# Optimization experiments

Hardware: AMD Instinct MI355X
Metric: run time of the kernel (lower is better)

Reference implementation:

```python
import jax, jax.numpy as jnp
import numpy as np

# Problem dims (match init_kwargs)
M, P, TINI, NH, TT, NB = 4, 6, 50, 100, 2000, 4096
L = TT - TINI - NH + 1  # 1851, dimension of g
NC = TINI * M + TINI * P + P  # 506 equality constraints
DELTA = 1e-6  # tiny ridge on g so the KKT system is nonsingular (u,y unchanged to ~1e-6)


def block_hankel(w, Lr, d):
    """w: flat [T*d] time series (d-dim samples stacked). Returns [Lr*d, T-Lr+1].
    H[d*i+k, j] = w[d*(i+j)+k] = w[row + d*j]."""
    T = w.shape[0] // d
    cols = T - Lr + 1
    return w[jnp.arange(Lr * d)[:, None] + d * jnp.arange(cols)[None, :]]


def setup_inputs() -> dict:
    key = jax.random.key(0)
    ks = jax.random.split(key, 7)
    ud = jax.random.normal(ks[0], (TT, M), jnp.float32)          # input data series
    yd = jax.random.normal(ks[1], (TT, P), jnp.float32)          # output data series
    q = 10.0 + 0.1 * jax.random.normal(ks[2], (P * NH,), jnp.float32)  # diag of Q (positive)
    r = 10.0 + 0.1 * jax.random.normal(ks[3], (M * NH,), jnp.float32)  # diag of R (positive)
    ref = jax.random.normal(ks[4], (NB, NH * P), jnp.float32)
    u_ini = jax.random.normal(ks[5], (NB, TINI * M), jnp.float32)
    y_ini = jax.random.normal(ks[6], (NB, TINI * P), jnp.float32)
    return {"ud": ud, "yd": yd, "q": q, "r": r, "ref": ref, "u_ini": u_ini, "y_ini": y_ini}


def reference(ud, yd, q, r, ref, u_ini, y_ini):
    # Block-Hankel data matrices (the module's U, Y Parameters)
    U = block_hankel(ud.reshape(-1), TINI + NH, M)  # [(Tini+N)*m, L]
    Y = block_hankel(yd.reshape(-1), TINI + NH, P)  # [(Tini+N)*p, L]
    Up, Uf = U[: M * TINI], U[M * TINI:]            # [Tini*m, L], [N*m, L]
    Yp, Yf = Y[: P * TINI], Y[P * TINI:]            # [Tini*p, L], [N*p, L]

    # Deterministic (linear, non-stochastic) DeePC QP with inactive box constraints:
    #   min_g (Yf g - ref)^T Q (Yf g - ref) + (Uf g)^T R (Uf g)
    #   s.t.  Up g = u_ini, Yp g = y_ini, (Yf g)[-p:] = ref[-p:]
    # Solved exactly via the KKT system (unique in u = Uf g, y = Yf g).
    H = Yf.T @ (q[:, None] * Yf) + Uf.T @ (r[:, None] * Uf) + DELTA * jnp.eye(L, dtype=ud.dtype)
    A = jnp.concatenate([Up, Yp, Yf[-P:]], axis=0)  # [NC, L]
    KKT = jnp.block([
        [2.0 * H, A.T],
        [A, jnp.zeros((NC, NC), dtype=ud.dtype)],
    ])  # [L+NC, L+NC]

    rhs = jnp.concatenate([
        2.0 * (Yf.T @ (q[:, None] * ref.T)),  # [L, NB] gradient term
        u_ini.T,                               # [Tini*m, NB]
        y_ini.T,                               # [Tini*p, NB]
        ref[:, -P:].T,                          # [p, NB] terminal constraint
    ], axis=0)

    g = jnp.linalg.solve(KKT, rhs)[:L]  # [L, NB]
    inp = Uf @ g   # optimal input  [N*m, NB]
    out = Yf @ g   # optimal output [N*p, NB]
    return inp, out
```

## Files before the change

kernel.cpp:

```cpp
#include <hip/hip_runtime.h>
#include <hip/hip_bf16.h>

#define LDIM   1851
#define NFR    1000
#define NAR    506
#define NCRP   1536
#define LDC    1856
#define NG     1024
#define NS     512
#define NXC    1152
#define LDMA   1120
#define NBATCH 4096
#define NOUT   1000
#define INVDP  500000.0

#define OFF_C     ((size_t)0)
#define SZ_C      ((size_t)NCRP * LDC * 4)
#define OFF_ILG   OFF_C
#define OFF_ILS   (OFF_C + 8388608)
#define OFF_GCC   (OFF_C + SZ_C)
#define SZ_GCC    ((size_t)NCRP * NCRP * 8)
#define OFF_G     (OFF_GCC + SZ_GCC)
#define SZ_G      ((size_t)NG * NG * 8)
#define OFF_TA    (OFF_G + SZ_G)
#define SZ_TA     ((size_t)NG * NS * 8)
#define OFF_S     (OFF_TA + SZ_TA)
#define SZ_S      ((size_t)NS * NS * 8)
#define OFF_X12   (OFF_S + SZ_S)
#define SZ_X12    ((size_t)NS * NXC * 8)
#define OFF_MRAW  (OFF_X12 + SZ_X12)
#define SZ_MRAW   ((size_t)NG * NXC * 4)
#define OFF_XB    OFF_MRAW
#define OFF_MALL  (OFF_MRAW + SZ_MRAW)
#define SZ_MALL   ((size_t)NG * LDMA * 4)
#define OFF_IDG   OFF_MALL
#define OFF_IDS   (OFF_MALL + 524288)
#define OFF_WG    (OFF_MALL + 786432)
#define OFF_WS    (OFF_MALL + 1310720)
#define OFF_LS    (OFF_MALL + 1572864)
#define OFF_INALL (OFF_MALL + SZ_MALL)
#define SZ_INALL  ((size_t)LDMA * NBATCH * 4)
#define OFF_TB    OFF_INALL
#define OFF_TINV  (OFF_INALL + 4194304)
#define OFF_LG    (OFF_INALL + 6291456)

__device__ __forceinline__ double dweight(int i, const float* q, const float* r) {
  return (i < 400) ? (double)r[i] : (double)q[i - 400];
}

__global__ __launch_bounds__(256) void k_build_C(const float* __restrict__ ud,
                                                 const float* __restrict__ yd,
                                                 float* __restrict__ C) {
  int j = blockIdx.x * 256 + threadIdx.x;
  int rr = blockIdx.y;
  if (j >= LDC) return;
  float v = 0.f;
  if (j < LDIM) {
    if (rr < 400)        v = ud[200 + rr + 4 * j];
    else if (rr < 1000)  v = yd[300 + (rr - 400) + 6 * j];
    else if (rr < 1200)  v = ud[(rr - 1000) + 4 * j];
    else if (rr < 1500)  v = yd[(rr - 1200) + 6 * j];
    else if (rr < 1506)  v = yd[894 + (rr - 1500) + 6 * j];
  }
  C[(size_t)rr * LDC + j] = v;
}

__global__ __launch_bounds__(256) void k_gram(const float* __restrict__ C,
                                              double* __restrict__ GCC) {
  int ti = blockIdx.y;
  int tj = blockIdx.x;
  if (ti * 32 + 31 < tj * 64) return;
  __shared__ float As[32][33];
  __shared__ float Bs[64][33];
  int tid = threadIdx.x;
  int tr2 = (tid >> 4) * 2, tc4 = (tid & 15) * 4;
  double acc[2][4] = {};
  int i0 = ti * 32, j0 = tj * 64;
  for (int k0 = 0; k0 < LDC; k0 += 32) {
#pragma unroll
    for (int l = 0; l < 4; ++l) {
      int t = tid + l * 256;
      As[t >> 5][t & 31] = C[(size_t)(i0 + (t >> 5)) * LDC + k0 + (t & 31)];
    }
#pragma unroll
    for (int l = 0; l < 8; ++l) {
      int t = tid + l * 256;
      Bs[t >> 5][t & 31] = C[(size_t)(j0 + (t >> 5)) * LDC + k0 + (t & 31)];
    }
    __syncthreads();
#pragma unroll
    for (int kk = 0; kk < 32; ++kk) {
      double a[2], b[4];
#pragma unroll
      for (int i = 0; i < 2; ++i) a[i] = (double)As[tr2 + i][kk];
#pragma unroll
      for (int jx = 0; jx < 4; ++jx) b[jx] = (double)Bs[tc4 + jx][kk];
#pragma unroll
      for (int i = 0; i < 2; ++i)
#pragma unroll
        for (int jx = 0; jx < 4; ++jx) acc[i][jx] += a[i] * b[jx];
    }
    __syncthreads();
  }
#pragma unroll
  for (int i = 0; i < 2; ++i)
#pragma unroll
    for (int jx = 0; jx < 4; ++jx) {
      int gi = i0 + tr2 + i, gj = j0 + tc4 + jx;
      GCC[(size_t)gi * NCRP + gj] = acc[i][jx];
      if (gi > gj) GCC[(size_t)gj * NCRP + gi] = acc[i][jx];
    }
}

__global__ __launch_bounds__(256) void k_copyG(const double* __restrict__ GCC,
                                               const float* __restrict__ q,
                                               const float* __restrict__ r,
                                               double* __restrict__ G) {
  int idx = blockIdx.x * 256 + threadIdx.x;
  int i = idx >> 10, j = idx & 1023;
  double v = (i < NFR && j < NFR) ? GCC[(size_t)i * NCRP + j] : 0.0;
  if (i == j) {
    if (i < NFR) v += 1e-6 / dweight(i, q, r);
    else v = 1.0;
  }
  G[idx] = v;
}

__global__ __launch_bounds__(256) void k_copyTA(const double* __restrict__ GCC,
                                                double* __restrict__ TA) {
  int idx = blockIdx.x * 256 + threadIdx.x;
  int f = idx >> 9, a = idx & 511;
  TA[idx] = (f < NFR && a < NAR) ? GCC[(size_t)f * NCRP + 1000 + a] : 0.0;
}

__device__ __forceinline__ void potrf_inv_w(double* sm, int tid,
                                            double* Ldst, int ld,
                                            double* iLout, double* Wout) {
  double* invd = sm + 4160;
  for (int c = 0; c < 64; ++c) {
    if (tid == 0) sm[c * 65 + c] = sqrt(sm[c * 65 + c]);
    __syncthreads();
    double piv = sm[c * 65 + c];
    for (int rr = c + 1 + tid; rr < 64; rr += 256) sm[rr * 65 + c] /= piv;
    __syncthreads();
    for (int t = tid; t < 64 * 64; t += 256) {
      int rr = t >> 6, jj = t & 63;
      if (rr > c && jj > c) sm[rr * 65 + jj] -= sm[rr * 65 + c] * sm[jj * 65 + c];
    }
    __syncthreads();
  }
#pragma unroll
  for (int l = 0; l < 16; ++l) {
    int t = tid + l * 256;
    Ldst[(size_t)(t >> 6) * ld + (t & 63)] = sm[(t >> 6) * 65 + (t & 63)];
  }
  __syncthreads();
  if (tid < 64) invd[tid] = 1.0 / sm[tid * 65 + tid];
  __syncthreads();
  if (tid < 64) {
    int c = tid;
    for (int r = c + 1; r < 64; ++r) {
      double s = sm[r * 65 + c] * invd[c];
      for (int j = c + 1; j < r; ++j) s += sm[r * 65 + j] * sm[c * 65 + j];
      sm[c * 65 + r] = -s * invd[r];
    }
  }
  __syncthreads();
#pragma unroll
  for (int l = 0; l < 16; ++l) {
    int t = tid + l * 256;
    int r = t >> 6, c = t & 63;
    iLout[t] = (r < c) ? 0.0 : (r == c ? invd[r] : sm[c * 65 + r]);
  }
  for (int idx = tid; idx < 4096; idx += 256) {
    int r = idx >> 6, c = idx & 63;
    int k2 = r > c ? r : c;
    double s = 0.0;
    for (; k2 < 64; ++k2) {
      double ar = (k2 == r) ? invd[r] : sm[r * 65 + k2];
      double ac = (k2 == c) ? invd[c] : sm[c * 65 + k2];
      s += ar * ac;
    }
    Wout[idx] = s;
  }
}

__global__ __launch_bounds__(256) void k_potrf_inv0(double* __restrict__ M, int ld,
                                                    double* __restrict__ LG,
                                                    double* __restrict__ iL0,
                                                    double* __restrict__ W0) {
  __shared__ double sm[4160 + 64];
  int tid = threadIdx.x;
#pragma unroll
  for (int l = 0; l < 16; ++l) {
    int t = tid + l * 256;
    sm[(t >> 6) * 65 + (t & 63)] = M[(size_t)(t >> 6) * ld + (t & 63)];
  }
  __syncthreads();
  potrf_inv_w(sm, tid, LG, ld, iL0, W0);
}

#define FS1(r, c) sm[(r) * 65 + (c)]
#define FS2(r, c) sm[4160 + (r) * 33 + (c)]
__global__ __launch_bounds__(256) void k_chol_fused(double* __restrict__ M, int ld, int k,
                                                    const double* __restrict__ iLcur,
                                                    const double* __restrict__ Wcur,
                                                    double* __restrict__ LG,
                                                    double* __restrict__ iLnext,
                                                    double* __restrict__ Wnext) {
  __shared__ double sm[6272];
  int tid = threadIdx.x;
  int t = blockIdx.x;
  int i = (int)((sqrtf(8.f * t + 1.f) - 1.f) * 0.5f);
  while ((i + 1) * (i + 2) / 2 <= t) ++i;
  while (i * (i + 1) / 2 > t) --i;
  int j = t - i * (i + 1) / 2;
  int tr4 = (tid >> 4) * 4, tc4 = (tid & 15) * 4;
  int rowAi = k + 64 + i * 64, rowAj = k + 64 + j * 64;

  if (j == 0) {
#pragma unroll
    for (int l = 0; l < 16; ++l) { int t2 = tid + l * 256; FS1(t2 >> 6, t2 & 63) = iLcur[t2]; }
    __syncthreads();
    double li[4][4] = {};
    for (int k0 = 0; k0 < 64; k0 += 32) {
#pragma unroll
      for (int l = 0; l < 8; ++l) {
        int t2 = tid + l * 256;
        FS2(t2 >> 5, t2 & 31) = M[(size_t)(rowAi + (t2 >> 5)) * ld + k + k0 + (t2 & 31)];
      }
      __syncthreads();
#pragma unroll
      for (int mm = 0; mm < 32; ++mm) {
        double a[4], b[4];
#pragma unroll
        for (int i2 = 0; i2 < 4; ++i2) a[i2] = FS2(tr4 + i2, mm);
#pragma unroll
        for (int j2 = 0; j2 < 4; ++j2) b[j2] = FS1(tc4 + j2, k0 + mm);
#pragma unroll
        for (int i2 = 0; i2 < 4; ++i2)
#pragma unroll
          for (int j2 = 0; j2 < 4; ++j2) li[i2][j2] += a[i2] * b[j2];
      }
      __syncthreads();
    }
#pragma unroll
    for (int i2 = 0; i2 < 4; ++i2)
#pragma unroll
      for (int j2 = 0; j2 < 4; ++j2)
        LG[(size_t)(rowAi + tr4 + i2) * ld + k + tc4 + j2] = li[i2][j2];
  }
  __syncthreads();

#pragma unroll
  for (int l = 0; l < 16; ++l) { int t2 = tid + l * 256; FS1(t2 >> 6, t2 & 63) = Wcur[t2]; }
  __syncthreads();
  double acc[4][4] = {};
  for (int k0 = 0; k0 < 64; k0 += 32) {
#pragma unroll
    for (int l = 0; l < 8; ++l) {
      int t2 = tid + l * 256;
      FS2(t2 >> 5, t2 & 31) = M[(size_t)(rowAj + (t2 >> 5)) * ld + k + k0 + (t2 & 31)];
    }
    __syncthreads();
#pragma unroll
    for (int mm = 0; mm < 32; ++mm) {
      double a[4], b[4];
#pragma unroll
      for (int i2 = 0; i2 < 4; ++i2) a[i2] = FS1(tr4 + i2, k0 + mm);
#pragma unroll
      for (int j2 = 0; j2 < 4; ++j2) b[j2] = FS2(tc4 + j2, mm);
#pragma unroll
      for (int i2 = 0; i2 < 4; ++i2)
#pragma unroll
        for (int j2 = 0; j2 < 4; ++j2) acc[i2][j2] += a[i2] * b[j2];
    }
    __syncthreads();
  }
#pragma unroll
  for (int i2 = 0; i2 < 4; ++i2)
#pragma unroll
    for (int j2 = 0; j2 < 4; ++j2) FS1(tr4 + i2, tc4 + j2) = acc[i2][j2];
  __syncthreads();
  double acc2[4][4] = {};
  for (int k0 = 0; k0 < 64; k0 += 32) {
#pragma unroll
    for (int l = 0; l < 8; ++l) {
      int t2 = tid + l * 256;
      FS2(t2 >> 5, t2 & 31) = M[(size_t)(rowAi + (t2 >> 5)) * ld + k + k0 + (t2 & 31)];
    }
    __syncthreads();
#pragma unroll
    for (int mm = 0; mm < 32; ++mm) {
      double a[4], b[4];
#pragma unroll
      for (int i2 = 0; i2 < 4; ++i2) a[i2] = FS2(tr4 + i2, mm);
#pragma unroll
      for (int j2 = 0; j2 < 4; ++j2) b[j2] = FS1(k0 + mm, tc4 + j2);
#pragma unroll
      for (int i2 = 0; i2 < 4; ++i2)
#pragma unroll
        for (int j2 = 0; j2 < 4; ++j2) acc2[i2][j2] += a[i2] * b[j2];
    }
    __syncthreads();
  }
  double upd[4][4];
#pragma unroll
  for (int i2 = 0; i2 < 4; ++i2)
#pragma unroll
    for (int j2 = 0; j2 < 4; ++j2) {
      size_t off = (size_t)(rowAi + tr4 + i2) * ld + rowAj + tc4 + j2;
      upd[i2][j2] = M[off] - acc2[i2][j2];
      M[off] = upd[i2][j2];
    }

  if (blockIdx.x == 0) {
    __syncthreads();
#pragma unroll
    for (int i2 = 0; i2 < 4; ++i2)
#pragma unroll
      for (int j2 = 0; j2 < 4; ++j2) FS1(tr4 + i2, tc4 + j2) = upd[i2][j2];
    __syncthreads();
    potrf_inv_w(sm, tid, LG + (size_t)(k + 64) * ld + (k + 64), ld, iLnext, Wnext);
  }
}

__device__ __forceinline__ void dgemm_nn_core(const double* __restrict__ A, int lda,
                                              const double* __restrict__ B, int ldb,
                                              double* __restrict__ C, int ldc,
                                              int kBeg, int kEnd, double alpha) {
  __shared__ double As[64][33];
  __shared__ double Bs[32][65];
  int tid = threadIdx.x;
  int tr4 = (tid >> 4) * 4, tc4 = (tid & 15) * 4;
  double acc[4][4] = {};
  for (int k0 = kBeg; k0 < kEnd; k0 += 32) {
#pragma unroll
    for (int l = 0; l < 8; ++l) {
      int t = tid + l * 256;
      As[t >> 5][t & 31] = A[(size_t)(t >> 5) * lda + k0 + (t & 31)];
    }
#pragma unroll
    for (int l = 0; l < 8; ++l) {
      int t = tid + l * 256;
      Bs[t >> 6][t & 63] = B[(size_t)(k0 + (t >> 6)) * ldb + (t & 63)];
    }
    __syncthreads();
#pragma unroll
    for (int kk = 0; kk < 32; ++kk) {
      double a[4], b[4];
#pragma unroll
      for (int i = 0; i < 4; ++i) a[i] = As[tr4 + i][kk];
#pragma unroll
      for (int jx = 0; jx < 4; ++jx) b[jx] = Bs[kk][tc4 + jx];
#pragma unroll
      for (int i = 0; i < 4; ++i)
#pragma unroll
        for (int jx = 0; jx < 4; ++jx) acc[i][jx] += a[i] * b[jx];
    }
    __syncthreads();
  }
#pragma unroll
  for (int i = 0; i < 4; ++i)
#pragma unroll
    for (int jx = 0; jx < 4; ++jx)
      C[(size_t)(tr4 + i) * ldc + tc4 + jx] = alpha * acc[i][jx];
}

__device__ __forceinline__ void dgemm_tn_core(const double* __restrict__ A, int lda,
                                              const double* __restrict__ B, int ldb,
                                              double* __restrict__ C, int ldc,
                                              int kBeg, int kEnd, double alpha) {
  __shared__ double Ls[32][65];
  __shared__ double Bs[32][65];
  int tid = threadIdx.x;
  int tr4 = (tid >> 4) * 4, tc4 = (tid & 15) * 4;
  double acc[4][4] = {};
  for (int k0 = kBeg; k0 < kEnd; k0 += 32) {
#pragma unroll
    for (int l = 0; l < 8; ++l) {
      int t = tid + l * 256;
      int jj = t >> 6, rr = t & 63;
      Ls[jj][rr] = A[(size_t)(k0 + jj) * lda + rr];
    }
#pragma unroll
    for (int l = 0; l < 8; ++l) {
      int t = tid + l * 256;
      Bs[t >> 6][t & 63] = B[(size_t)(k0 + (t >> 6)) * ldb + (t & 63)];
    }
    __syncthreads();
#pragma unroll
    for (int kk = 0; kk < 32; ++kk) {
      double a[4], b[4];
#pragma unroll
      for (int i = 0; i < 4; ++i) a[i] = Ls[kk][tr4 + i];
#pragma unroll
      for (int jx = 0; jx < 4; ++jx) b[jx] = Bs[kk][tc4 + jx];
#pragma unroll
      for (int i = 0; i < 4; ++i)
#pragma unroll
        for (int jx = 0; jx < 4; ++jx) acc[i][jx] += a[i] * b[jx];
    }
    __syncthreads();
  }
#pragma unroll
  for (int i = 0; i < 4; ++i)
#pragma unroll
    for (int jx = 0; jx < 4; ++jx)
      C[(size_t)(tr4 + i) * ldc + tc4 + jx] = alpha * acc[i][jx];
}

__global__ __launch_bounds__(256) void k_dgemm_nn(const double* __restrict__ A, int lda,
                                                  const double* __restrict__ B, int ldb,
                                                  double* __restrict__ C, int ldc,
                                                  int K, int tri, double alpha) {
  int bi = blockIdx.y, bj = blockIdx.x;
  int kEnd = tri ? ((bi + 1) * 64 < K ? (bi + 1) * 64 : K) : K;
  dgemm_nn_core(A + (size_t)bi * 64 * lda, lda, B + bj * 64, ldb,
                C + (size_t)bi * 64 * ldc + bj * 64, ldc, 0, kEnd, alpha);
}

__global__ __launch_bounds__(256) void k_dgemm_tn(const double* __restrict__ A, int lda,
                                                  const double* __restrict__ B, int ldb,
                                                  double* __restrict__ C, int ldc,
                                                  int K, int tri, double alpha) {
  int bi = blockIdx.y, bj = blockIdx.x;
  int kBeg = tri ? bi * 64 : 0;
  dgemm_tn_core(A + bi * 64, lda, B + bj * 64, ldb,
                C + (size_t)bi * 64 * ldc + bj * 64, ldc, kBeg, K, alpha);
}

__global__ __launch_bounds__(256) void k_init_iL(double* __restrict__ iL, int nShift,
                                                 const double* __restrict__ IDIAG) {
  int idx = blockIdx.x * 256 + threadIdx.x;
  int n = 1 << nShift;
  int i = idx >> nShift, j = idx & (n - 1);
  int d = i >> 6;
  double v = 0.0;
  if ((j >> 6) == d) v = IDIAG[(size_t)d * 4096 + (i & 63) * 64 + (j & 63)];
  iL[idx] = v;
}

__global__ __launch_bounds__(256) void k_ilv_tmp(const double* __restrict__ L, int ldl,
                                                 const double* __restrict__ iL, int ldi,
                                                 double* __restrict__ T, int half) {
  int p = blockIdx.z, bi = blockIdx.y, bj = blockIdx.x;
  int base = p * 2 * half;
  dgemm_nn_core(L + (size_t)(base + half + bi * 64) * ldl + base, ldl,
                iL + (size_t)base * ldi + base + bj * 64, ldi,
                T + (size_t)p * half * half + (size_t)bi * 64 * half + bj * 64, half,
                0, half, 1.0);
}

__global__ __launch_bounds__(256) void k_ilv_fin(double* __restrict__ iL, int ldi,
                                                 const double* __restrict__ T, int half) {
  int p = blockIdx.z, bi = blockIdx.y, bj = blockIdx.x;
  int base = p * 2 * half;
  dgemm_nn_core(iL + (size_t)(base + half + bi * 64) * ldi + base + half, ldi,
                T + (size_t)p * half * half + bj * 64, half,
                iL + (size_t)(base + half + bi * 64) * ldi + base + bj * 64, ldi,
                0, half, -1.0);
}

__global__ __launch_bounds__(256) void k_buildS(const double* __restrict__ GCC,
                                                const double* __restrict__ TA,
                                                double* __restrict__ S) {
  __shared__ double Ga[64][33];
  __shared__ double Tb[32][65];
  int tid = threadIdx.x;
  int tr4 = (tid >> 4) * 4, tc4 = (tid & 15) * 4;
  int a0 = blockIdx.y * 64, b0 = blockIdx.x * 64;
  double acc[4][4] = {};
  for (int f0 = 0; f0 < NG; f0 += 32) {
#pragma unroll
    for (int l = 0; l < 8; ++l) {
      int t = tid + l * 256;
      Ga[t >> 5][t & 31] = GCC[(size_t)(1000 + a0 + (t >> 5)) * NCRP + f0 + (t & 31)];
    }
#pragma unroll
    for (int l = 0; l < 8; ++l) {
      int t = tid + l * 256;
      Tb[t >> 6][t & 63] = TA[(size_t)(f0 + (t >> 6)) * NS + b0 + (t & 63)];
    }
    __syncthreads();
#pragma unroll
    for (int kk = 0; kk < 32; ++kk) {
      double a[4], b[4];
#pragma unroll
      for (int i = 0; i < 4; ++i) a[i] = Ga[tr4 + i][kk];
#pragma unroll
      for (int jx = 0; jx < 4; ++jx) b[jx] = Tb[kk][tc4 + jx];
#pragma unroll
      for (int i = 0; i < 4; ++i)
#pragma unroll
        for (int jx = 0; jx < 4; ++jx) acc[i][jx] += a[i] * b[jx];
    }
    __syncthreads();
  }
#pragma unroll
  for (int i = 0; i < 4; ++i)
#pragma unroll
    for (int jx = 0; jx < 4; ++jx) {
      int a = a0 + tr4 + i, b = b0 + tc4 + jx;
      double v;
      if (a < NAR && b < NAR)
        v = (GCC[(size_t)(1000 + a) * NCRP + 1000 + b] - acc[i][jx]) * INVDP;
      else
        v = (a == b) ? 1.0 : 0.0;
      S[(size_t)a * NS + b] = v;
    }
}

__global__ __launch_bounds__(256) void k_build_x12rhs(const double* __restrict__ TA,
                                                      double* __restrict__ X12) {
  int c = blockIdx.x * 256 + threadIdx.x;
  int a = blockIdx.y;
  if (c >= NXC) return;
  double v = 0.0;
  if (a < NAR) {
    if (c < 600) v = TA[(size_t)(400 + c) * NS + a];
    else if (c < 1106) v = (a == (c - 600)) ? 1.0 : 0.0;
  }
  X12[(size_t)a * NXC + c] = v;
}

__global__ __launch_bounds__(256) void k_gemm_M(const double* __restrict__ TA,
                                                const double* __restrict__ X12,
                                                const float* __restrict__ q,
                                                const float* __restrict__ r,
                                                float* __restrict__ Mraw) {
  __shared__ double Ga[64][33];
  __shared__ double Xb[32][65];
  int tid = threadIdx.x;
  int tr4 = (tid >> 4) * 4, tc4 = (tid & 15) * 4;
  int o0 = blockIdx.y * 64, c0 = blockIdx.x * 64;
  double acc[4][4] = {};
  for (int k0 = 0; k0 < NS; k0 += 32) {
#pragma unroll
    for (int l = 0; l < 8; ++l) {
      int t = tid + l * 256;
      Ga[t >> 5][t & 31] = TA[(size_t)(o0 + (t >> 5)) * NS + k0 + (t & 31)];
    }
#pragma unroll
    for (int l = 0; l < 8; ++l) {
      int t = tid + l * 256;
      Xb[t >> 6][t & 63] = X12[(size_t)(k0 + (t >> 6)) * NXC + c0 + (t & 63)];
    }
    __syncthreads();
#pragma unroll
    for (int kk = 0; kk < 32; ++kk) {
      double a[4], b[4];
#pragma unroll
      for (int i = 0; i < 4; ++i) a[i] = Ga[tr4 + i][kk];
#pragma unroll
      for (int jx = 0; jx < 4; ++jx) b[jx] = Xb[kk][tc4 + jx];
#pragma unroll
      for (int i = 0; i < 4; ++i)
#pragma unroll
        for (int jx = 0; jx < 4; ++jx) acc[i][jx] += a[i] * b[jx];
    }
    __syncthreads();
  }
#pragma unroll
  for (int i = 0; i < 4; ++i)
#pragma unroll
    for (int jx = 0; jx < 4; ++jx) {
      int o = o0 + tr4 + i, col = c0 + tc4 + jx;
      float v = 0.f;
      if (o < NFR) {
        double scale = 1.0 / (2.0 * dweight(o, q, r));
        double tt = acc[i][jx] * scale;
        v = (float)((col < 600) ? -tt : tt);
      }
      Mraw[(size_t)o * NXC + col] = v;
    }
}

__global__ __launch_bounds__(256) void k_assemble_M(const float* __restrict__ Mraw,
                                                    float* __restrict__ Mall) {
  int j = blockIdx.x * 256 + threadIdx.x;
  int o = blockIdx.y;
  if (j >= LDMA) return;
  float v = 0.f;
  if (j < 600) {
    v = Mraw[(size_t)o * NXC + j];
    if (o == 400 + j) v += 1.0f;
    if (j >= 594) v += Mraw[(size_t)o * NXC + 1100 + (j - 594)];
  } else if (j < 1100) {
    v = Mraw[(size_t)o * NXC + j];
  }
  Mall[(size_t)o * LDMA + j] = v;
}

__global__ __launch_bounds__(256) void k_transpose_in(const float* __restrict__ ref,
                                                      const float* __restrict__ ui,
                                                      const float* __restrict__ yi,
                                                      float* __restrict__ INall) {
  __shared__ float t[32][33];
  int tx = threadIdx.x & 31, ty = threadIdx.x >> 5;
  int n0 = blockIdx.x * 32, j0 = blockIdx.y * 32;
#pragma unroll
  for (int p = 0; p < 4; ++p) {
    int nb = n0 + ty + p * 8;
    int j = j0 + tx;
    float v = 0.f;
    if (j < 600)        v = ref[(size_t)nb * 600 + j];
    else if (j < 800)   v = ui[(size_t)nb * 200 + (j - 600)];
    else if (j < 1100)  v = yi[(size_t)nb * 300 + (j - 800)];
    t[ty + p * 8][tx] = v;
  }
  __syncthreads();
#pragma unroll
  for (int p = 0; p < 4; ++p) {
    INall[(size_t)(j0 + ty + p * 8) * NBATCH + n0 + tx] = t[tx][ty + p * 8];
  }
}

__global__ __launch_bounds__(256) void k_gemm_out(const float* __restrict__ Mall,
                                                  const float* __restrict__ INall,
                                                  float* __restrict__ out) {
  __shared__ float As[32][132];
  __shared__ float Bs[32][132];
  int tid = threadIdx.x;
  int tr = tid >> 4, tc = tid & 15;
  int m0 = blockIdx.y * 128, n0 = blockIdx.x * 128;
  float acc[8][8] = {};
  for (int k0 = 0; k0 < LDMA; k0 += 32) {
#pragma unroll
    for (int l = 0; l < 16; ++l) {
      int t = tid + l * 256;
      int rr = t >> 5, cc = t & 31;
      As[cc][rr] = Mall[(size_t)(m0 + rr) * LDMA + k0 + cc];
    }
#pragma unroll
    for (int l = 0; l < 16; ++l) {
      int t = tid + l * 256;
      int rr = t >> 7, cc = t & 127;
      Bs[rr][cc] = INall[(size_t)(k0 + rr) * NBATCH + n0 + cc];
    }
    __syncthreads();
#pragma unroll
    for (int kk = 0; kk < 32; ++kk) {
      float4 a0 = *(const float4*)&As[kk][tr * 4];
      float4 a1 = *(const float4*)&As[kk][64 + tr * 4];
      float4 b0 = *(const float4*)&Bs[kk][tc * 4];
      float4 b1 = *(const float4*)&Bs[kk][64 + tc * 4];
      float av[8] = {a0.x, a0.y, a0.z, a0.w, a1.x, a1.y, a1.z, a1.w};
      float bv[8] = {b0.x, b0.y, b0.z, b0.w, b1.x, b1.y, b1.z, b1.w};
#pragma unroll
      for (int i = 0; i < 8; ++i)
#pragma unroll
        for (int jx = 0; jx < 8; ++jx) acc[i][jx] += av[i] * bv[jx];
    }
    __syncthreads();
  }
#pragma unroll
  for (int ih = 0; ih < 2; ++ih)
#pragma unroll
    for (int i = 0; i < 4; ++i) {
      int o = m0 + ih * 64 + tr * 4 + i;
      if (o < NOUT) {
#pragma unroll
        for (int jh = 0; jh < 2; ++jh) {
          float4 v = make_float4(acc[ih * 4 + i][jh * 4 + 0], acc[ih * 4 + i][jh * 4 + 1],
                                 acc[ih * 4 + i][jh * 4 + 2], acc[ih * 4 + i][jh * 4 + 3]);
          *(float4*)&out[(size_t)o * NBATCH + n0 + jh * 64 + tc * 4] = v;
        }
      }
    }
}

extern "C" void kernel_launch(void* const* d_in, const int* in_sizes, int n_in,
                              void* d_out, int out_size, void* d_ws, size_t ws_size,
                              hipStream_t stream) {
  const float* ud  = (const float*)d_in[0];
  const float* yd  = (const float*)d_in[1];
  const float* qv  = (const float*)d_in[2];
  const float* rv  = (const float*)d_in[3];
  const float* ref = (const float*)d_in[4];
  const float* ui  = (const float*)d_in[5];
  const float* yi  = (const float*)d_in[6];
  float* out = (float*)d_out;
  char* w = (char*)d_ws;

  float*  C    = (float*)(w + OFF_C);
  double* GCC  = (double*)(w + OFF_GCC);
  double* G    = (double*)(w + OFF_G);
  double* TA   = (double*)(w + OFF_TA);
  double* S    = (double*)(w + OFF_S);
  double* X12  = (double*)(w + OFF_X12);
  float*  MRAW = (float*)(w + OFF_MRAW);
  float*  MALL = (float*)(w + OFF_MALL);
  float*  INA  = (float*)(w + OFF_INALL);
  double* ILG  = (double*)(w + OFF_ILG);
  double* ILS  = (double*)(w + OFF_ILS);
  double* IDG  = (double*)(w + OFF_IDG);
  double* IDS  = (double*)(w + OFF_IDS);
  double* WG   = (double*)(w + OFF_WG);
  double* WS   = (double*)(w + OFF_WS);
  double* LG   = (double*)(w + OFF_LG);
  double* LS   = (double*)(w + OFF_LS);
  double* TB   = (double*)(w + OFF_TB);
  double* TINV = (double*)(w + OFF_TINV);
  double* XB   = (double*)(w + OFF_XB);

  k_build_C<<<dim3(8, NCRP), 256, 0, stream>>>(ud, yd, C);
  k_gram<<<dim3(24, 48), 256, 0, stream>>>(C, GCC);
  k_copyG<<<dim3(NG * NG / 256), 256, 0, stream>>>(GCC, qv, rv, G);
  k_copyTA<<<dim3(NG * NS / 256), 256, 0, stream>>>(GCC, TA);

  k_potrf_inv0<<<1, 256, 0, stream>>>(G, NG, LG, IDG, WG);
  for (int p = 0; p < 15; ++p) {
    int nb = 15 - p;
    k_chol_fused<<<dim3(nb * (nb + 1) / 2), 256, 0, stream>>>(
        G, NG, p * 64, IDG + (size_t)p * 4096, WG + (size_t)p * 4096, LG,
        IDG + (size_t)(p + 1) * 4096, WG + (size_t)(p + 1) * 4096);
  }

  k_init_iL<<<dim3(NG * NG / 256), 256, 0, stream>>>(ILG, 10, IDG);
  for (int lv = 0; lv < 4; ++lv) {
    int half = 64 << lv, pairs = NG / (2 * half);
    dim3 gt(half / 64, half / 64, pairs);
    k_ilv_tmp<<<gt, 256, 0, stream>>>(LG, NG, ILG, NG, TINV, half);
    k_ilv_fin<<<gt, 256, 0, stream>>>(ILG, NG, TINV, half);
  }
  k_dgemm_nn<<<dim3(NS / 64, NG / 64), 256, 0, stream>>>(ILG, NG, TA, NS, TB, NS, NG, 1, 1.0);
  k_dgemm_tn<<<dim3(NS / 64, NG / 64), 256, 0, stream>>>(ILG, NG, TB, NS, TA, NS, NG, 1, 1.0);

  k_buildS<<<dim3(8, 8), 256, 0, stream>>>(GCC, TA, S);
  k_potrf_inv0<<<1, 256, 0, stream>>>(S, NS, LS, IDS, WS);
  for (int p = 0; p < 7; ++p) {
    int nb = 7 - p;
    k_chol_fused<<<dim3(nb * (nb + 1) / 2), 256, 0, stream>>>(
        S, NS, p * 64, IDS + (size_t)p * 4096, WS + (size_t)p * 4096, LS,
        IDS + (size_t)(p + 1) * 4096, WS + (size_t)(p + 1) * 4096);
  }
  k_init_iL<<<dim3(NS * NS / 256), 256, 0, stream>>>(ILS, 9, IDS);
  for (int lv = 0; lv < 3; ++lv) {
    int half = 64 << lv, pairs = NS / (2 * half);
    dim3 gt(half / 64, half / 64, pairs);
    k_ilv_tmp<<<gt, 256, 0, stream>>>(LS, NS, ILS, NS, TINV, half);
    k_ilv_fin<<<gt, 256, 0, stream>>>(ILS, NS, TINV, half);
  }

  k_build_x12rhs<<<dim3(5, NS), 256, 0, stream>>>(TA, X12);
  k_dgemm_nn<<<dim3(NXC / 64, NS / 64), 256, 0, stream>>>(ILS, NS, X12, NXC, XB, NXC, NS, 1, 1.0);
  k_dgemm_tn<<<dim3(NXC / 64, NS / 64), 256, 0, stream>>>(ILS, NS, XB, NXC, X12, NXC, NS, 1, 1.0);

  k_gemm_M<<<dim3(NXC / 64, NG / 64), 256, 0, stream>>>(TA, X12, qv, rv, MRAW);
  k_assemble_M<<<dim3(5, NG), 256, 0, stream>>>(MRAW, MALL);
  k_transpose_in<<<dim3(NBATCH / 32, LDMA / 32), 256, 0, stream>>>(ref, ui, yi, INA);
  k_gemm_out<<<dim3(NBATCH / 128, NG / 128), 256, 0, stream>>>(MALL, INA, out);
}
```

Measured before the change: 5.889 ms.

## Fuse factorization pipeline into one persistent kernel with grid barriers

Replaces roughly forty small sequential launches (copy, blocked Cholesky panels, triangular inverse levels, GEMMs, assembly) with a single persistent kernel of 240 blocks that walks the stages and separates them with an atomic-counter grid barrier. The aim is to remove per-launch overhead and tail gaps between tiny kernels. The Gram kernel also moves to square 64x64 tiles. The barrier relies on all 240 blocks being co-resident without a cooperative launch, which risks deadlock if occupancy is insufficient, and many stages leave most blocks idle while they spin.

```diff
diff --git a/kernel.cpp b/kernel.cpp
--- a/kernel.cpp
+++ b/kernel.cpp
@@ -13,11 +13,13 @@
 #define NBATCH 4096
 #define NOUT   1000
 #define INVDP  500000.0
+#define NBLK   240
 
 #define OFF_C     ((size_t)0)
 #define SZ_C      ((size_t)NCRP * LDC * 4)
 #define OFF_ILG   OFF_C
 #define OFF_ILS   (OFF_C + 8388608)
+#define OFF_BAR   (OFF_C + 10485760)
 #define OFF_GCC   (OFF_C + SZ_C)
 #define SZ_GCC    ((size_t)NCRP * NCRP * 8)
 #define OFF_G     (OFF_GCC + SZ_GCC)
@@ -48,6 +50,21 @@
   return (i < 400) ? (double)r[i] : (double)q[i - 400];
 }
 
+__device__ __forceinline__ void gbar(unsigned int* cnt, unsigned int* phase) {
+  __syncthreads();
+  __threadfence();
+  if (threadIdx.x == 0) {
+    unsigned int target = (++(*phase)) * (unsigned int)gridDim.x;
+    __hip_atomic_fetch_add(cnt, 1u, __ATOMIC_RELEASE, __HIP_MEMORY_SCOPE_AGENT);
+    while (__hip_atomic_load(cnt, __ATOMIC_ACQUIRE, __HIP_MEMORY_SCOPE_AGENT) < target) {
+      __builtin_amdgcn_s_sleep(2);
+    }
+  }
+  __threadfence();
+  __syncthreads();
+}
+
+
 __global__ __launch_bounds__(256) void k_build_C(const float* __restrict__ ud,
                                                  const float* __restrict__ yd,
                                                  float* __restrict__ C) {
@@ -67,292 +84,30 @@
 
 __global__ __launch_bounds__(256) void k_gram(const float* __restrict__ C,
                                               double* __restrict__ GCC) {
-  int ti = blockIdx.y;
-  int tj = blockIdx.x;
-  if (ti * 32 + 31 < tj * 64) return;
-  __shared__ float As[32][33];
+  int ti = blockIdx.y, tj = blockIdx.x;
+  if (ti < tj) return;
+  __shared__ float As[64][33];
   __shared__ float Bs[64][33];
-  int tid = threadIdx.x;
-  int tr2 = (tid >> 4) * 2, tc4 = (tid & 15) * 4;
-  double acc[2][4] = {};
-  int i0 = ti * 32, j0 = tj * 64;
-  for (int k0 = 0; k0 < LDC; k0 += 32) {
-#pragma unroll
-    for (int l = 0; l < 4; ++l) {
-      int t = tid + l * 256;
-      As[t >> 5][t & 31] = C[(size_t)(i0 + (t >> 5)) * LDC + k0 + (t & 31)];
-    }
-#pragma unroll
-    for (int l = 0; l < 8; ++l) {
-      int t = tid + l * 256;
-      Bs[t >> 5][t & 31] = C[(size_t)(j0 + (t >> 5)) * LDC + k0 + (t & 31)];
-    }
-    __syncthreads();
-#pragma unroll
-    for (int kk = 0; kk < 32; ++kk) {
-      double a[2], b[4];
-#pragma unroll
-      for (int i = 0; i < 2; ++i) a[i] = (double)As[tr2 + i][kk];
-#pragma unroll
-      for (int jx = 0; jx < 4; ++jx) b[jx] = (double)Bs[tc4 + jx][kk];
-#pragma unroll
-      for (int i = 0; i < 2; ++i)
-#pragma unroll
-        for (int jx = 0; jx < 4; ++jx) acc[i][jx] += a[i] * b[jx];
-    }
-    __syncthreads();
-  }
-#pragma unroll
-  for (int i = 0; i < 2; ++i)
-#pragma unroll
-    for (int jx = 0; jx < 4; ++jx) {
-      int gi = i0 + tr2 + i, gj = j0 + tc4 + jx;
-      GCC[(size_t)gi * NCRP + gj] = acc[i][jx];
-      if (gi > gj) GCC[(size_t)gj * NCRP + gi] = acc[i][jx];
-    }
-}
-
-__global__ __launch_bounds__(256) void k_copyG(const double* __restrict__ GCC,
-                                               const float* __restrict__ q,
-                                               const float* __restrict__ r,
-                                               double* __restrict__ G) {
-  int idx = blockIdx.x * 256 + threadIdx.x;
-  int i = idx >> 10, j = idx & 1023;
-  double v = (i < NFR && j < NFR) ? GCC[(size_t)i * NCRP + j] : 0.0;
-  if (i == j) {
-    if (i < NFR) v += 1e-6 / dweight(i, q, r);
-    else v = 1.0;
-  }
-  G[idx] = v;
-}
-
-__global__ __launch_bounds__(256) void k_copyTA(const double* __restrict__ GCC,
-                                                double* __restrict__ TA) {
-  int idx = blockIdx.x * 256 + threadIdx.x;
-  int f = idx >> 9, a = idx & 511;
-  TA[idx] = (f < NFR && a < NAR) ? GCC[(size_t)f * NCRP + 1000 + a] : 0.0;
-}
-
-__device__ __forceinline__ void potrf_inv_w(double* sm, int tid,
-                                            double* Ldst, int ld,
-                                            double* iLout, double* Wout) {
-  double* invd = sm + 4160;
-  for (int c = 0; c < 64; ++c) {
-    if (tid == 0) sm[c * 65 + c] = sqrt(sm[c * 65 + c]);
-    __syncthreads();
-    double piv = sm[c * 65 + c];
-    for (int rr = c + 1 + tid; rr < 64; rr += 256) sm[rr * 65 + c] /= piv;
-    __syncthreads();
-    for (int t = tid; t < 64 * 64; t += 256) {
-      int rr = t >> 6, jj = t & 63;
-      if (rr > c && jj > c) sm[rr * 65 + jj] -= sm[rr * 65 + c] * sm[jj * 65 + c];
-    }
-    __syncthreads();
-  }
-#pragma unroll
-  for (int l = 0; l < 16; ++l) {
-    int t = tid + l * 256;
-    Ldst[(size_t)(t >> 6) * ld + (t & 63)] = sm[(t >> 6) * 65 + (t & 63)];
-  }
-  __syncthreads();
-  if (tid < 64) invd[tid] = 1.0 / sm[tid * 65 + tid];
-  __syncthreads();
-  if (tid < 64) {
-    int c = tid;
-    for (int r = c + 1; r < 64; ++r) {
-      double s = sm[r * 65 + c] * invd[c];
-      for (int j = c + 1; j < r; ++j) s += sm[r * 65 + j] * sm[c * 65 + j];
-      sm[c * 65 + r] = -s * invd[r];
-    }
-  }
-  __syncthreads();
-#pragma unroll
-  for (int l = 0; l < 16; ++l) {
-    int t = tid + l * 256;
-    int r = t >> 6, c = t & 63;
-    iLout[t] = (r < c) ? 0.0 : (r == c ? invd[r] : sm[c * 65 + r]);
-  }
-  for (int idx = tid; idx < 4096; idx += 256) {
-    int r = idx >> 6, c = idx & 63;
-    int k2 = r > c ? r : c;
-    double s = 0.0;
-    for (; k2 < 64; ++k2) {
-      double ar = (k2 == r) ? invd[r] : sm[r * 65 + k2];
-      double ac = (k2 == c) ? invd[c] : sm[c * 65 + k2];
-      s += ar * ac;
-    }
-    Wout[idx] = s;
-  }
-}
-
-__global__ __launch_bounds__(256) void k_potrf_inv0(double* __restrict__ M, int ld,
-                                                    double* __restrict__ LG,
-                                                    double* __restrict__ iL0,
-                                                    double* __restrict__ W0) {
-  __shared__ double sm[4160 + 64];
-  int tid = threadIdx.x;
-#pragma unroll
-  for (int l = 0; l < 16; ++l) {
-    int t = tid + l * 256;
-    sm[(t >> 6) * 65 + (t & 63)] = M[(size_t)(t >> 6) * ld + (t & 63)];
-  }
-  __syncthreads();
-  potrf_inv_w(sm, tid, LG, ld, iL0, W0);
-}
-
-#define FS1(r, c) sm[(r) * 65 + (c)]
-#define FS2(r, c) sm[4160 + (r) * 33 + (c)]
-__global__ __launch_bounds__(256) void k_chol_fused(double* __restrict__ M, int ld, int k,
-                                                    const double* __restrict__ iLcur,
-                                                    const double* __restrict__ Wcur,
-                                                    double* __restrict__ LG,
-                                                    double* __restrict__ iLnext,
-                                                    double* __restrict__ Wnext) {
-  __shared__ double sm[6272];
-  int tid = threadIdx.x;
-  int t = blockIdx.x;
-  int i = (int)((sqrtf(8.f * t + 1.f) - 1.f) * 0.5f);
-  while ((i + 1) * (i + 2) / 2 <= t) ++i;
-  while (i * (i + 1) / 2 > t) --i;
-  int j = t - i * (i + 1) / 2;
-  int tr4 = (tid >> 4) * 4, tc4 = (tid & 15) * 4;
-  int rowAi = k + 64 + i * 64, rowAj = k + 64 + j * 64;
-
-  if (j == 0) {
-#pragma unroll
-    for (int l = 0; l < 16; ++l) { int t2 = tid + l * 256; FS1(t2 >> 6, t2 & 63) = iLcur[t2]; }
-    __syncthreads();
-    double li[4][4] = {};
-    for (int k0 = 0; k0 < 64; k0 += 32) {
-#pragma unroll
-      for (int l = 0; l < 8; ++l) {
-        int t2 = tid + l * 256;
-        FS2(t2 >> 5, t2 & 31) = M[(size_t)(rowAi + (t2 >> 5)) * ld + k + k0 + (t2 & 31)];
-      }
-      __syncthreads();
-#pragma unroll
-      for (int mm = 0; mm < 32; ++mm) {
-        double a[4], b[4];
-#pragma unroll
-        for (int i2 = 0; i2 < 4; ++i2) a[i2] = FS2(tr4 + i2, mm);
-#pragma unroll
-        for (int j2 = 0; j2 < 4; ++j2) b[j2] = FS1(tc4 + j2, k0 + mm);
-#pragma unroll
-        for (int i2 = 0; i2 < 4; ++i2)
-#pragma unroll
-          for (int j2 = 0; j2 < 4; ++j2) li[i2][j2] += a[i2] * b[j2];
-      }
-      __syncthreads();
-    }
-#pragma unroll
-    for (int i2 = 0; i2 < 4; ++i2)
-#pragma unroll
-      for (int j2 = 0; j2 < 4; ++j2)
-        LG[(size_t)(rowAi + tr4 + i2) * ld + k + tc4 + j2] = li[i2][j2];
-  }
-  __syncthreads();
-
-#pragma unroll
-  for (int l = 0; l < 16; ++l) { int t2 = tid + l * 256; FS1(t2 >> 6, t2 & 63) = Wcur[t2]; }
-  __syncthreads();
-  double acc[4][4] = {};
-  for (int k0 = 0; k0 < 64; k0 += 32) {
-#pragma unroll
-    for (int l = 0; l < 8; ++l) {
-      int t2 = tid + l * 256;
-      FS2(t2 >> 5, t2 & 31) = M[(size_t)(rowAj + (t2 >> 5)) * ld + k + k0 + (t2 & 31)];
-    }
-    __syncthreads();
-#pragma unroll
-    for (int mm = 0; mm < 32; ++mm) {
-      double a[4], b[4];
-#pragma unroll
-      for (int i2 = 0; i2 < 4; ++i2) a[i2] = FS1(tr4 + i2, k0 + mm);
-#pragma unroll
-      for (int j2 = 0; j2 < 4; ++j2) b[j2] = FS2(tc4 + j2, mm);
-#pragma unroll
-      for (int i2 = 0; i2 < 4; ++i2)
-#pragma unroll
-        for (int j2 = 0; j2 < 4; ++j2) acc[i2][j2] += a[i2] * b[j2];
-    }
-    __syncthreads();
-  }
-#pragma unroll
-  for (int i2 = 0; i2 < 4; ++i2)
-#pragma unroll
-    for (int j2 = 0; j2 < 4; ++j2) FS1(tr4 + i2, tc4 + j2) = acc[i2][j2];
-  __syncthreads();
-  double acc2[4][4] = {};
-  for (int k0 = 0; k0 < 64; k0 += 32) {
-#pragma unroll
-    for (int l = 0; l < 8; ++l) {
-      int t2 = tid + l * 256;
-      FS2(t2 >> 5, t2 & 31) = M[(size_t)(rowAi + (t2 >> 5)) * ld + k + k0 + (t2 & 31)];
-    }
-    __syncthreads();
-#pragma unroll
-    for (int mm = 0; mm < 32; ++mm) {
-      double a[4], b[4];
-#pragma unroll
-      for (int i2 = 0; i2 < 4; ++i2) a[i2] = FS2(tr4 + i2, mm);
-#pragma unroll
-      for (int j2 = 0; j2 < 4; ++j2) b[j2] = FS1(k0 + mm, tc4 + j2);
-#pragma unroll
-      for (int i2 = 0; i2 < 4; ++i2)
-#pragma unroll
-        for (int j2 = 0; j2 < 4; ++j2) acc2[i2][j2] += a[i2] * b[j2];
-    }
-    __syncthreads();
-  }
-  double upd[4][4];
-#pragma unroll
-  for (int i2 = 0; i2 < 4; ++i2)
-#pragma unroll
-    for (int j2 = 0; j2 < 4; ++j2) {
-      size_t off = (size_t)(rowAi + tr4 + i2) * ld + rowAj + tc4 + j2;
-      upd[i2][j2] = M[off] - acc2[i2][j2];
-      M[off] = upd[i2][j2];
-    }
-
-  if (blockIdx.x == 0) {
-    __syncthreads();
-#pragma unroll
-    for (int i2 = 0; i2 < 4; ++i2)
-#pragma unroll
-      for (int j2 = 0; j2 < 4; ++j2) FS1(tr4 + i2, tc4 + j2) = upd[i2][j2];
-    __syncthreads();
-    potrf_inv_w(sm, tid, LG + (size_t)(k + 64) * ld + (k + 64), ld, iLnext, Wnext);
-  }
-}
-
-__device__ __forceinline__ void dgemm_nn_core(const double* __restrict__ A, int lda,
-                                              const double* __restrict__ B, int ldb,
-                                              double* __restrict__ C, int ldc,
-                                              int kBeg, int kEnd, double alpha) {
-  __shared__ double As[64][33];
-  __shared__ double Bs[32][65];
   int tid = threadIdx.x;
   int tr4 = (tid >> 4) * 4, tc4 = (tid & 15) * 4;
   double acc[4][4] = {};
-  for (int k0 = kBeg; k0 < kEnd; k0 += 32) {
+  int i0 = ti * 64, j0 = tj * 64;
+  for (int k0 = 0; k0 < LDC; k0 += 32) {
 #pragma unroll
     for (int l = 0; l < 8; ++l) {
       int t = tid + l * 256;
-      As[t >> 5][t & 31] = A[(size_t)(t >> 5) * lda + k0 + (t & 31)];
-    }
-#pragma unroll
-    for (int l = 0; l < 8; ++l) {
-      int t = tid + l * 256;
-      Bs[t >> 6][t & 63] = B[(size_t)(k0 + (t >> 6)) * ldb + (t & 63)];
+      int rr = t >> 5, cc = t & 31;
+      As[rr][cc] = C[(size_t)(i0 + rr) * LDC + k0 + cc];
+      Bs[rr][cc] = C[(size_t)(j0 + rr) * LDC + k0 + cc];
     }
     __syncthreads();
 #pragma unroll
     for (int kk = 0; kk < 32; ++kk) {
       double a[4], b[4];
 #pragma unroll
-      for (int i = 0; i < 4; ++i) a[i] = As[tr4 + i][kk];
-#pragma unroll
-      for (int jx = 0; jx < 4; ++jx) b[jx] = Bs[kk][tc4 + jx];
+      for (int i = 0; i < 4; ++i) a[i] = (double)As[tr4 + i][kk];
+#pragma unroll
+      for (int jx = 0; jx < 4; ++jx) b[jx] = (double)Bs[tc4 + jx][kk];
 #pragma unroll
       for (int i = 0; i < 4; ++i)
 #pragma unroll
@@ -363,233 +118,11 @@
 #pragma unroll
   for (int i = 0; i < 4; ++i)
 #pragma unroll
-    for (int jx = 0; jx < 4; ++jx)
-      C[(size_t)(tr4 + i) * ldc + tc4 + jx] = alpha * acc[i][jx];
-}
-
-__device__ __forceinline__ void dgemm_tn_core(const double* __restrict__ A, int lda,
-                                              const double* __restrict__ B, int ldb,
-                                              double* __restrict__ C, int ldc,
-                                              int kBeg, int kEnd, double alpha) {
-  __shared__ double Ls[32][65];
-  __shared__ double Bs[32][65];
-  int tid = threadIdx.x;
-  int tr4 = (tid >> 4) * 4, tc4 = (tid & 15) * 4;
-  double acc[4][4] = {};
-  for (int k0 = kBeg; k0 < kEnd; k0 += 32) {
-#pragma unroll
-    for (int l = 0; l < 8; ++l) {
-      int t = tid + l * 256;
-      int jj = t >> 6, rr = t & 63;
-      Ls[jj][rr] = A[(size_t)(k0 + jj) * lda + rr];
-    }
-#pragma unroll
-    for (int l = 0; l < 8; ++l) {
-      int t = tid + l * 256;
-      Bs[t >> 6][t & 63] = B[(size_t)(k0 + (t >> 6)) * ldb + (t & 63)];
-    }
-    __syncthreads();
-#pragma unroll
-    for (int kk = 0; kk < 32; ++kk) {
-      double a[4], b[4];
-#pragma unroll
-      for (int i = 0; i < 4; ++i) a[i] = Ls[kk][tr4 + i];
-#pragma unroll
-      for (int jx = 0; jx < 4; ++jx) b[jx] = Bs[kk][tc4 + jx];
-#pragma unroll
-      for (int i = 0; i < 4; ++i)
-#pragma unroll
-        for (int jx = 0; jx < 4; ++jx) acc[i][jx] += a[i] * b[jx];
-    }
-    __syncthreads();
-  }
-#pragma unroll
-  for (int i = 0; i < 4; ++i)
-#pragma unroll
-    for (int jx = 0; jx < 4; ++jx)
-      C[(size_t)(tr4 + i) * ldc + tc4 + jx] = alpha * acc[i][jx];
-}
-
-__global__ __launch_bounds__(256) void k_dgemm_nn(const double* __restrict__ A, int lda,
-                                                  const double* __restrict__ B, int ldb,
-                                                  double* __restrict__ C, int ldc,
-                                                  int K, int tri, double alpha) {
-  int bi = blockIdx.y, bj = blockIdx.x;
-  int kEnd = tri ? ((bi + 1) * 64 < K ? (bi + 1) * 64 : K) : K;
-  dgemm_nn_core(A + (size_t)bi * 64 * lda, lda, B + bj * 64, ldb,
-                C + (size_t)bi * 64 * ldc + bj * 64, ldc, 0, kEnd, alpha);
-}
-
-__global__ __launch_bounds__(256) void k_dgemm_tn(const double* __restrict__ A, int lda,
-                                                  const double* __restrict__ B, int ldb,
-                                                  double* __restrict__ C, int ldc,
-                                                  int K, int tri, double alpha) {
-  int bi = blockIdx.y, bj = blockIdx.x;
-  int kBeg = tri ? bi * 64 : 0;
-  dgemm_tn_core(A + bi * 64, lda, B + bj * 64, ldb,
-                C + (size_t)bi * 64 * ldc + bj * 64, ldc, kBeg, K, alpha);
-}
-
-__global__ __launch_bounds__(256) void k_init_iL(double* __restrict__ iL, int nShift,
-                                                 const double* __restrict__ IDIAG) {
-  int idx = blockIdx.x * 256 + threadIdx.x;
-  int n = 1 << nShift;
-  int i = idx >> nShift, j = idx & (n - 1);
-  int d = i >> 6;
-  double v = 0.0;
-  if ((j >> 6) == d) v = IDIAG[(size_t)d * 4096 + (i & 63) * 64 + (j & 63)];
-  iL[idx] = v;
-}
-
-__global__ __launch_bounds__(256) void k_ilv_tmp(const double* __restrict__ L, int ldl,
-                                                 const double* __restrict__ iL, int ldi,
-                                                 double* __restrict__ T, int half) {
-  int p = blockIdx.z, bi = blockIdx.y, bj = blockIdx.x;
-  int base = p * 2 * half;
-  dgemm_nn_core(L + (size_t)(base + half + bi * 64) * ldl + base, ldl,
-                iL + (size_t)base * ldi + base + bj * 64, ldi,
-                T + (size_t)p * half * half + (size_t)bi * 64 * half + bj * 64, half,
-                0, half, 1.0);
-}
-
-__global__ __launch_bounds__(256) void k_ilv_fin(double* __restrict__ iL, int ldi,
-                                                 const double* __restrict__ T, int half) {
-  int p = blockIdx.z, bi = blockIdx.y, bj = blockIdx.x;
-  int base = p * 2 * half;
-  dgemm_nn_core(iL + (size_t)(base + half + bi * 64) * ldi + base + half, ldi,
-                T + (size_t)p * half * half + bj * 64, half,
-                iL + (size_t)(base + half + bi * 64) * ldi + base + bj * 64, ldi,
-                0, half, -1.0);
-}
-
-__global__ __launch_bounds__(256) void k_buildS(const double* __restrict__ GCC,
-                                                const double* __restrict__ TA,
-                                                double* __restrict__ S) {
-  __shared__ double Ga[64][33];
-  __shared__ double Tb[32][65];
-  int tid = threadIdx.x;
-  int tr4 = (tid >> 4) * 4, tc4 = (tid & 15) * 4;
-  int a0 = blockIdx.y * 64, b0 = blockIdx.x * 64;
-  double acc[4][4] = {};
-  for (int f0 = 0; f0 < NG; f0 += 32) {
-#pragma unroll
-    for (int l = 0; l < 8; ++l) {
-      int t = tid + l * 256;
-      Ga[t >> 5][t & 31] = GCC[(size_t)(1000 + a0 + (t >> 5)) * NCRP + f0 + (t & 31)];
-    }
-#pragma unroll
-    for (int l = 0; l < 8; ++l) {
-      int t = tid + l * 256;
-      Tb[t >> 6][t & 63] = TA[(size_t)(f0 + (t >> 6)) * NS + b0 + (t & 63)];
-    }
-    __syncthreads();
-#pragma unroll
-    for (int kk = 0; kk < 32; ++kk) {
-      double a[4], b[4];
-#pragma unroll
-      for (int i = 0; i < 4; ++i) a[i] = Ga[tr4 + i][kk];
-#pragma unroll
-      for (int jx = 0; jx < 4; ++jx) b[jx] = Tb[kk][tc4 + jx];
-#pragma unroll
-      for (int i = 0; i < 4; ++i)
-#pragma unroll
-        for (int jx = 0; jx < 4; ++jx) acc[i][jx] += a[i] * b[jx];
-    }
-    __syncthreads();
-  }
-#pragma unroll
-  for (int i = 0; i < 4; ++i)
-#pragma unroll
     for (int jx = 0; jx < 4; ++jx) {
-      int a = a0 + tr4 + i, b = b0 + tc4 + jx;
-      double v;
-      if (a < NAR && b < NAR)
-        v = (GCC[(size_t)(1000 + a) * NCRP + 1000 + b] - acc[i][jx]) * INVDP;
-      else
-        v = (a == b) ? 1.0 : 0.0;
-      S[(size_t)a * NS + b] = v;
-    }
-}
-
-__global__ __launch_bounds__(256) void k_build_x12rhs(const double* __restrict__ TA,
-                                                      double* __restrict__ X12) {
-  int c = blockIdx.x * 256 + threadIdx.x;
-  int a = blockIdx.y;
-  if (c >= NXC) return;
-  double v = 0.0;
-  if (a < NAR) {
-    if (c < 600) v = TA[(size_t)(400 + c) * NS + a];
-    else if (c < 1106) v = (a == (c - 600)) ? 1.0 : 0.0;
-  }
-  X12[(size_t)a * NXC + c] = v;
-}
-
-__global__ __launch_bounds__(256) void k_gemm_M(const double* __restrict__ TA,
-                                                const double* __restrict__ X12,
-                                                const float* __restrict__ q,
-                                                const float* __restrict__ r,
-                                                float* __restrict__ Mraw) {
-  __shared__ double Ga[64][33];
-  __shared__ double Xb[32][65];
-  int tid = threadIdx.x;
-  int tr4 = (tid >> 4) * 4, tc4 = (tid & 15) * 4;
-  int o0 = blockIdx.y * 64, c0 = blockIdx.x * 64;
-  double acc[4][4] = {};
-  for (int k0 = 0; k0 < NS; k0 += 32) {
-#pragma unroll
-    for (int l = 0; l < 8; ++l) {
-      int t = tid + l * 256;
-      Ga[t >> 5][t & 31] = TA[(size_t)(o0 + (t >> 5)) * NS + k0 + (t & 31)];
-    }
-#pragma unroll
-    for (int l = 0; l < 8; ++l) {
-      int t = tid + l * 256;
-      Xb[t >> 6][t & 63] = X12[(size_t)(k0 + (t >> 6)) * NXC + c0 + (t & 63)];
-    }
-    __syncthreads();
-#pragma unroll
-    for (int kk = 0; kk < 32; ++kk) {
-      double a[4], b[4];
-#pragma unroll
-      for (int i = 0; i < 4; ++i) a[i] = Ga[tr4 + i][kk];
-#pragma unroll
-      for (int jx = 0; jx < 4; ++jx) b[jx] = Xb[kk][tc4 + jx];
-#pragma unroll
-      for (int i = 0; i < 4; ++i)
-#pragma unroll
-        for (int jx = 0; jx < 4; ++jx) acc[i][jx] += a[i] * b[jx];
-    }
-    __syncthreads();
-  }
-#pragma unroll
-  for (int i = 0; i < 4; ++i)
-#pragma unroll
-    for (int jx = 0; jx < 4; ++jx) {
-      int o = o0 + tr4 + i, col = c0 + tc4 + jx;
-      float v = 0.f;
-      if (o < NFR) {
-        double scale = 1.0 / (2.0 * dweight(o, q, r));
-        double tt = acc[i][jx] * scale;
-        v = (float)((col < 600) ? -tt : tt);
-      }
-      Mraw[(size_t)o * NXC + col] = v;
-    }
-}
-
-__global__ __launch_bounds__(256) void k_assemble_M(const float* __restrict__ Mraw,
-                                                    float* __restrict__ Mall) {
-  int j = blockIdx.x * 256 + threadIdx.x;
-  int o = blockIdx.y;
-  if (j >= LDMA) return;
-  float v = 0.f;
-  if (j < 600) {
-    v = Mraw[(size_t)o * NXC + j];
-    if (o == 400 + j) v += 1.0f;
-    if (j >= 594) v += Mraw[(size_t)o * NXC + 1100 + (j - 594)];
-  } else if (j < 1100) {
-    v = Mraw[(size_t)o * NXC + j];
-  }
-  Mall[(size_t)o * LDMA + j] = v;
+      int gi = i0 + tr4 + i, gj = j0 + tc4 + jx;
+      GCC[(size_t)gi * NCRP + gj] = acc[i][jx];
+      if (ti != tj) GCC[(size_t)gj * NCRP + gi] = acc[i][jx];
+    }
 }
 
 __global__ __launch_bounds__(256) void k_transpose_in(const float* __restrict__ ref,
@@ -667,6 +200,534 @@
           *(float4*)&out[(size_t)o * NBATCH + n0 + jh * 64 + tc * 4] = v;
         }
       }
+    }
+}
+
+
+__device__ __forceinline__ void potrf_inv_w(double* sm, int tid,
+                                            double* Ldst, int ld,
+                                            double* iLout, double* Wout) {
+  double* invd = sm + 4160;
+  for (int c = 0; c < 64; ++c) {
+    if (tid == 0) sm[c * 65 + c] = sqrt(sm[c * 65 + c]);
+    __syncthreads();
+    double piv = sm[c * 65 + c];
+    for (int rr = c + 1 + tid; rr < 64; rr += 256) sm[rr * 65 + c] /= piv;
+    __syncthreads();
+    for (int t = tid; t < 64 * 64; t += 256) {
+      int rr = t >> 6, jj = t & 63;
+      if (rr > c && jj > c) sm[rr * 65 + jj] -= sm[rr * 65 + c] * sm[jj * 65 + c];
+    }
+    __syncthreads();
+  }
+#pragma unroll
+  for (int l = 0; l < 16; ++l) {
+    int t = tid + l * 256;
+    Ldst[(size_t)(t >> 6) * ld + (t & 63)] = sm[(t >> 6) * 65 + (t & 63)];
+  }
+  __syncthreads();
+  if (tid < 64) invd[tid] = 1.0 / sm[tid * 65 + tid];
+  __syncthreads();
+  if (tid < 64) {
+    int c = tid;
+    for (int r = c + 1; r < 64; ++r) {
+      double s = sm[r * 65 + c] * invd[c];
+      for (int j = c + 1; j < r; ++j) s += sm[r * 65 + j] * sm[c * 65 + j];
+      sm[c * 65 + r] = -s * invd[r];
+    }
+  }
+  __syncthreads();
+#pragma unroll
+  for (int l = 0; l < 16; ++l) {
+    int t = tid + l * 256;
+    int r = t >> 6, c = t & 63;
+    iLout[t] = (r < c) ? 0.0 : (r == c ? invd[r] : sm[c * 65 + r]);
+  }
+  for (int idx = tid; idx < 4096; idx += 256) {
+    int r = idx >> 6, c = idx & 63;
+    int k2 = r > c ? r : c;
+    double s = 0.0;
+    for (; k2 < 64; ++k2) {
+      double ar = (k2 == r) ? invd[r] : sm[r * 65 + k2];
+      double ac = (k2 == c) ? invd[c] : sm[c * 65 + k2];
+      s += ar * ac;
+    }
+    Wout[idx] = s;
+  }
+}
+
+#define PFS1(r, c) sm[(r) * 65 + (c)]
+#define PFS2(r, c) sm[4288 + (r) * 33 + (c)]
+__device__ __forceinline__ void chol_panel(double* sm, double* M, int ld, int k, int nbp,
+                                           const double* iLcur, const double* Wcur,
+                                           double* LGm, double* iLnext, double* Wnext) {
+  int tid = threadIdx.x;
+  int t = blockIdx.x;
+  int tiles = nbp * (nbp + 1) / 2;
+  if (t >= tiles) return;
+  int i = 0;
+  while ((i + 1) * (i + 2) / 2 <= t) ++i;
+  int j = t - i * (i + 1) / 2;
+  int tr4 = (tid >> 4) * 4, tc4 = (tid & 15) * 4;
+  int rowAi = k + 64 + i * 64, rowAj = k + 64 + j * 64;
+
+  if (j == 0) {
+#pragma unroll
+    for (int l = 0; l < 16; ++l) { int t2 = tid + l * 256; PFS1(t2 >> 6, t2 & 63) = iLcur[t2]; }
+    __syncthreads();
+    double li[4][4] = {};
+    for (int k0 = 0; k0 < 64; k0 += 32) {
+#pragma unroll
+      for (int l = 0; l < 8; ++l) {
+        int t2 = tid + l * 256;
+        PFS2(t2 >> 5, t2 & 31) = M[(size_t)(rowAi + (t2 >> 5)) * ld + k + k0 + (t2 & 31)];
+      }
+      __syncthreads();
+#pragma unroll
+      for (int mm = 0; mm < 32; ++mm) {
+        double a[4], b[4];
+#pragma unroll
+        for (int i2 = 0; i2 < 4; ++i2) a[i2] = PFS2(tr4 + i2, mm);
+#pragma unroll
+        for (int j2 = 0; j2 < 4; ++j2) b[j2] = PFS1(tc4 + j2, k0 + mm);
+#pragma unroll
+        for (int i2 = 0; i2 < 4; ++i2)
+#pragma unroll
+          for (int j2 = 0; j2 < 4; ++j2) li[i2][j2] += a[i2] * b[j2];
+      }
+      __syncthreads();
+    }
+#pragma unroll
+    for (int i2 = 0; i2 < 4; ++i2)
+#pragma unroll
+      for (int j2 = 0; j2 < 4; ++j2)
+        LGm[(size_t)(rowAi + tr4 + i2) * ld + k + tc4 + j2] = li[i2][j2];
+  }
+  __syncthreads();
+
+#pragma unroll
+  for (int l = 0; l < 16; ++l) { int t2 = tid + l * 256; PFS1(t2 >> 6, t2 & 63) = Wcur[t2]; }
+  __syncthreads();
+  double acc[4][4] = {};
+  for (int k0 = 0; k0 < 64; k0 += 32) {
+#pragma unroll
+    for (int l = 0; l < 8; ++l) {
+      int t2 = tid + l * 256;
+      PFS2(t2 >> 5, t2 & 31) = M[(size_t)(rowAj + (t2 >> 5)) * ld + k + k0 + (t2 & 31)];
+    }
+    __syncthreads();
+#pragma unroll
+    for (int mm = 0; mm < 32; ++mm) {
+      double a[4], b[4];
+#pragma unroll
+      for (int i2 = 0; i2 < 4; ++i2) a[i2] = PFS1(tr4 + i2, k0 + mm);
+#pragma unroll
+      for (int j2 = 0; j2 < 4; ++j2) b[j2] = PFS2(tc4 + j2, mm);
+#pragma unroll
+      for (int i2 = 0; i2 < 4; ++i2)
+#pragma unroll
+        for (int j2 = 0; j2 < 4; ++j2) acc[i2][j2] += a[i2] * b[j2];
+    }
+    __syncthreads();
+  }
+#pragma unroll
+  for (int i2 = 0; i2 < 4; ++i2)
+#pragma unroll
+    for (int j2 = 0; j2 < 4; ++j2) PFS1(tr4 + i2, tc4 + j2) = acc[i2][j2];
+  __syncthreads();
+  double acc2[4][4] = {};
+  for (int k0 = 0; k0 < 64; k0 += 32) {
+#pragma unroll
+    for (int l = 0; l < 8; ++l) {
+      int t2 = tid + l * 256;
+      PFS2(t2 >> 5, t2 & 31) = M[(size_t)(rowAi + (t2 >> 5)) * ld + k + k0 + (t2 & 31)];
+    }
+    __syncthreads();
+#pragma unroll
+    for (int mm = 0; mm < 32; ++mm) {
+      double a[4], b[4];
+#pragma unroll
+      for (int i2 = 0; i2 < 4; ++i2) a[i2] = PFS2(tr4 + i2, mm);
+#pragma unroll
+      for (int j2 = 0; j2 < 4; ++j2) b[j2] = PFS1(k0 + mm, tc4 + j2);
+#pragma unroll
+      for (int i2 = 0; i2 < 4; ++i2)
+#pragma unroll
+        for (int j2 = 0; j2 < 4; ++j2) acc2[i2][j2] += a[i2] * b[j2];
+    }
+    __syncthreads();
+  }
+  double upd[4][4];
+#pragma unroll
+  for (int i2 = 0; i2 < 4; ++i2)
+#pragma unroll
+    for (int j2 = 0; j2 < 4; ++j2) {
+      size_t off = (size_t)(rowAi + tr4 + i2) * ld + rowAj + tc4 + j2;
+      upd[i2][j2] = M[off] - acc2[i2][j2];
+      M[off] = upd[i2][j2];
+    }
+
+  if (t == 0) {
+    __syncthreads();
+#pragma unroll
+    for (int i2 = 0; i2 < 4; ++i2)
+#pragma unroll
+      for (int j2 = 0; j2 < 4; ++j2) PFS1(tr4 + i2, tc4 + j2) = upd[i2][j2];
+    __syncthreads();
+    potrf_inv_w(sm, tid, LGm + (size_t)(k + 64) * ld + (k + 64), ld, iLnext, Wnext);
+  }
+}
+
+__device__ __forceinline__ void dgemm_nn_core(double* sm, const double* A, int lda,
+                                              const double* B, int ldb,
+                                              double* C, int ldc,
+                                              int kBeg, int kEnd, double alpha) {
+  double* As = sm;
+  double* Bs = sm + 2112;
+  int tid = threadIdx.x;
+  int tr4 = (tid >> 4) * 4, tc4 = (tid & 15) * 4;
+  double acc[4][4] = {};
+  for (int k0 = kBeg; k0 < kEnd; k0 += 32) {
+#pragma unroll
+    for (int l = 0; l < 8; ++l) {
+      int t = tid + l * 256;
+      As[(t >> 5) * 33 + (t & 31)] = A[(size_t)(t >> 5) * lda + k0 + (t & 31)];
+    }
+#pragma unroll
+    for (int l = 0; l < 8; ++l) {
+      int t = tid + l * 256;
+      Bs[(t >> 6) * 65 + (t & 63)] = B[(size_t)(k0 + (t >> 6)) * ldb + (t & 63)];
+    }
+    __syncthreads();
+#pragma unroll
+    for (int kk = 0; kk < 32; ++kk) {
+      double a[4], b[4];
+#pragma unroll
+      for (int i = 0; i < 4; ++i) a[i] = As[(tr4 + i) * 33 + kk];
+#pragma unroll
+      for (int jx = 0; jx < 4; ++jx) b[jx] = Bs[kk * 65 + tc4 + jx];
+#pragma unroll
+      for (int i = 0; i < 4; ++i)
+#pragma unroll
+        for (int jx = 0; jx < 4; ++jx) acc[i][jx] += a[i] * b[jx];
+    }
+    __syncthreads();
+  }
+#pragma unroll
+  for (int i = 0; i < 4; ++i)
+#pragma unroll
+    for (int jx = 0; jx < 4; ++jx)
+      C[(size_t)(tr4 + i) * ldc + tc4 + jx] = alpha * acc[i][jx];
+}
+
+__device__ __forceinline__ void dgemm_tn_core(double* sm, const double* A, int lda,
+                                              const double* B, int ldb,
+                                              double* C, int ldc,
+                                              int kBeg, int kEnd, double alpha) {
+  double* Ls = sm;
+  double* Bs = sm + 2080;
+  int tid = threadIdx.x;
+  int tr4 = (tid >> 4) * 4, tc4 = (tid & 15) * 4;
+  double acc[4][4] = {};
+  for (int k0 = kBeg; k0 < kEnd; k0 += 32) {
+#pragma unroll
+    for (int l = 0; l < 8; ++l) {
+      int t = tid + l * 256;
+      Ls[(t >> 6) * 65 + (t & 63)] = A[(size_t)(k0 + (t >> 6)) * lda + (t & 63)];
+    }
+#pragma unroll
+    for (int l = 0; l < 8; ++l) {
+      int t = tid + l * 256;
+      Bs[(t >> 6) * 65 + (t & 63)] = B[(size_t)(k0 + (t >> 6)) * ldb + (t & 63)];
+    }
+    __syncthreads();
+#pragma unroll
+    for (int kk = 0; kk < 32; ++kk) {
+      double a[4], b[4];
+#pragma unroll
+      for (int i = 0; i < 4; ++i) a[i] = Ls[kk * 65 + tr4 + i];
+#pragma unroll
+      for (int jx = 0; jx < 4; ++jx) b[jx] = Bs[kk * 65 + tc4 + jx];
+#pragma unroll
+      for (int i = 0; i < 4; ++i)
+#pragma unroll
+        for (int jx = 0; jx < 4; ++jx) acc[i][jx] += a[i] * b[jx];
+    }
+    __syncthreads();
+  }
+#pragma unroll
+  for (int i = 0; i < 4; ++i)
+#pragma unroll
+    for (int jx = 0; jx < 4; ++jx)
+      C[(size_t)(tr4 + i) * ldc + tc4 + jx] = alpha * acc[i][jx];
+}
+
+__device__ __forceinline__ void buildS_tile(double* sm, const double* GCC,
+                                            const double* TA, double* S, int t) {
+  double* Ga = sm;
+  double* Tb = sm + 2112;
+  int tid = threadIdx.x;
+  int tr4 = (tid >> 4) * 4, tc4 = (tid & 15) * 4;
+  int a0 = (t >> 3) * 64, b0 = (t & 7) * 64;
+  double acc[4][4] = {};
+  for (int f0 = 0; f0 < NG; f0 += 32) {
+#pragma unroll
+    for (int l = 0; l < 8; ++l) {
+      int t2 = tid + l * 256;
+      Ga[(t2 >> 5) * 33 + (t2 & 31)] = GCC[(size_t)(1000 + a0 + (t2 >> 5)) * NCRP + f0 + (t2 & 31)];
+    }
+#pragma unroll
+    for (int l = 0; l < 8; ++l) {
+      int t2 = tid + l * 256;
+      Tb[(t2 >> 6) * 65 + (t2 & 63)] = TA[(size_t)(f0 + (t2 >> 6)) * NS + b0 + (t2 & 63)];
+    }
+    __syncthreads();
+#pragma unroll
+    for (int kk = 0; kk < 32; ++kk) {
+      double a[4], b[4];
+#pragma unroll
+      for (int i = 0; i < 4; ++i) a[i] = Ga[(tr4 + i) * 33 + kk];
+#pragma unroll
+      for (int jx = 0; jx < 4; ++jx) b[jx] = Tb[kk * 65 + tc4 + jx];
+#pragma unroll
+      for (int i = 0; i < 4; ++i)
+#pragma unroll
+        for (int jx = 0; jx < 4; ++jx) acc[i][jx] += a[i] * b[jx];
+    }
+    __syncthreads();
+  }
+#pragma unroll
+  for (int i = 0; i < 4; ++i)
+#pragma unroll
+    for (int jx = 0; jx < 4; ++jx) {
+      int a = a0 + tr4 + i, b = b0 + tc4 + jx;
+      double v;
+      if (a < NAR && b < NAR)
+        v = (GCC[(size_t)(1000 + a) * NCRP + 1000 + b] - acc[i][jx]) * INVDP;
+      else
+        v = (a == b) ? 1.0 : 0.0;
+      S[(size_t)a * NS + b] = v;
+    }
+}
+
+__device__ __forceinline__ void gemmM_tile(double* sm, const double* TA, const double* X12,
+                                           const float* q, const float* r,
+                                           float* Mraw, int t) {
+  double* Ga = sm;
+  double* Xb = sm + 2112;
+  int tid = threadIdx.x;
+  int tr4 = (tid >> 4) * 4, tc4 = (tid & 15) * 4;
+  int o0 = (t / 18) * 64, c0 = (t % 18) * 64;
+  double acc[4][4] = {};
+  for (int k0 = 0; k0 < NS; k0 += 32) {
+#pragma unroll
+    for (int l = 0; l < 8; ++l) {
+      int t2 = tid + l * 256;
+      Ga[(t2 >> 5) * 33 + (t2 & 31)] = TA[(size_t)(o0 + (t2 >> 5)) * NS + k0 + (t2 & 31)];
+    }
+#pragma unroll
+    for (int l = 0; l < 8; ++l) {
+      int t2 = tid + l * 256;
+      Xb[(t2 >> 6) * 65 + (t2 & 63)] = X12[(size_t)(k0 + (t2 >> 6)) * NXC + c0 + (t2 & 63)];
+    }
+    __syncthreads();
+#pragma unroll
+    for (int kk = 0; kk < 32; ++kk) {
+      double a[4], b[4];
+#pragma unroll
+      for (int i = 0; i < 4; ++i) a[i] = Ga[(tr4 + i) * 33 + kk];
+#pragma unroll
+      for (int jx = 0; jx < 4; ++jx) b[jx] = Xb[kk * 65 + tc4 + jx];
+#pragma unroll
+      for (int i = 0; i < 4; ++i)
+#pragma unroll
+        for (int jx = 0; jx < 4; ++jx) acc[i][jx] += a[i] * b[jx];
+    }
+    __syncthreads();
+  }
+#pragma unroll
+  for (int i = 0; i < 4; ++i)
+#pragma unroll
+    for (int jx = 0; jx < 4; ++jx) {
+      int o = o0 + tr4 + i, col = c0 + tc4 + jx;
+      float v = 0.f;
+      if (o < NFR) {
+        double scale = 1.0 / (2.0 * dweight(o, q, r));
+        double tt = acc[i][jx] * scale;
+        v = (float)((col < 600) ? -tt : tt);
+      }
+      Mraw[(size_t)o * NXC + col] = v;
+    }
+}
+
+__global__ __launch_bounds__(256) void k_coop(
+    double* GCC, double* G, double* TA, double* S, double* X12,
+    float* MRAW, float* MALL,
+    double* ILG, double* ILS, double* IDG, double* IDS,
+    double* WG, double* WS, double* LG, double* LS,
+    double* TB, double* TINV, double* XB,
+    const float* qv, const float* rv, unsigned int* bar) {
+  __shared__ double sm[6400];
+  const int tid = threadIdx.x;
+  const int bid = blockIdx.x;
+  const int nbk = gridDim.x;
+  const int gsz = nbk * 256;
+  const int gix = bid * 256 + tid;
+  unsigned int phase = 0;
+
+  for (int idx = gix; idx < NG * NG; idx += gsz) {
+    int i = idx >> 10, j = idx & 1023;
+    double v = (i < NFR && j < NFR) ? GCC[(size_t)i * NCRP + j] : 0.0;
+    if (i == j) v = (i < NFR) ? v + 1e-6 / dweight(i, qv, rv) : 1.0;
+    G[idx] = v;
+  }
+  for (int idx = gix; idx < NG * NS; idx += gsz) {
+    int f = idx >> 9, a = idx & 511;
+    TA[idx] = (f < NFR && a < NAR) ? GCC[(size_t)f * NCRP + 1000 + a] : 0.0;
+  }
+  gbar(bar, &phase);
+
+  if (bid == 0) {
+    for (int l = 0; l < 16; ++l) {
+      int t2 = tid + l * 256;
+      sm[(t2 >> 6) * 65 + (t2 & 63)] = G[(size_t)(t2 >> 6) * NG + (t2 & 63)];
+    }
+    __syncthreads();
+    potrf_inv_w(sm, tid, LG, NG, IDG, WG);
+  }
+  gbar(bar, &phase);
+  for (int p = 0; p < 15; ++p) {
+    chol_panel(sm, G, NG, p * 64, 15 - p, IDG + (size_t)p * 4096, WG + (size_t)p * 4096,
+               LG, IDG + (size_t)(p + 1) * 4096, WG + (size_t)(p + 1) * 4096);
+    gbar(bar, &phase);
+  }
+
+  for (int idx = gix; idx < NG * NG; idx += gsz) {
+    int i = idx >> 10, j = idx & 1023;
+    int d = i >> 6;
+    ILG[idx] = ((j >> 6) == d) ? IDG[(size_t)d * 4096 + (i & 63) * 64 + (j & 63)] : 0.0;
+  }
+  gbar(bar, &phase);
+  for (int lv = 0; lv < 4; ++lv) {
+    int half = 64 << lv, pairs = NG / (2 * half), hb = half >> 6;
+    int tiles = pairs * hb * hb;
+    for (int t = bid; t < tiles; t += nbk) {
+      int p = t / (hb * hb), rem = t % (hb * hb), bi = rem / hb, bj = rem % hb;
+      int base = p * 2 * half;
+      dgemm_nn_core(sm, LG + (size_t)(base + half + bi * 64) * NG + base, NG,
+                    ILG + (size_t)base * NG + base + bj * 64, NG,
+                    TINV + (size_t)p * half * half + (size_t)bi * 64 * half + bj * 64, half,
+                    0, half, 1.0);
+    }
+    gbar(bar, &phase);
+    for (int t = bid; t < tiles; t += nbk) {
+      int p = t / (hb * hb), rem = t % (hb * hb), bi = rem / hb, bj = rem % hb;
+      int base = p * 2 * half;
+      dgemm_nn_core(sm, ILG + (size_t)(base + half + bi * 64) * NG + base + half, NG,
+                    TINV + (size_t)p * half * half + bj * 64, half,
+                    ILG + (size_t)(base + half + bi * 64) * NG + base + bj * 64, NG,
+                    0, half, -1.0);
+    }
+    gbar(bar, &phase);
+  }
+
+  for (int t = bid; t < 128; t += nbk) {
+    int bi = t >> 3, bj = t & 7;
+    dgemm_nn_core(sm, ILG + (size_t)bi * 64 * NG, NG, TA + bj * 64, NS,
+                  TB + (size_t)bi * 64 * NS + bj * 64, NS, 0, (bi + 1) * 64, 1.0);
+  }
+  gbar(bar, &phase);
+  for (int t = bid; t < 128; t += nbk) {
+    int bi = t >> 3, bj = t & 7;
+    dgemm_tn_core(sm, ILG + bi * 64, NG, TB + bj * 64, NS,
+                  TA + (size_t)bi * 64 * NS + bj * 64, NS, bi * 64, NG, 1.0);
+  }
+  gbar(bar, &phase);
+
+  for (int t = bid; t < 64; t += nbk) buildS_tile(sm, GCC, TA, S, t);
+  gbar(bar, &phase);
+
+  if (bid == 0) {
+    for (int l = 0; l < 16; ++l) {
+      int t2 = tid + l * 256;
+      sm[(t2 >> 6) * 65 + (t2 & 63)] = S[(size_t)(t2 >> 6) * NS + (t2 & 63)];
+    }
+    __syncthreads();
+    potrf_inv_w(sm, tid, LS, NS, IDS, WS);
+  }
+  gbar(bar, &phase);
+  for (int p = 0; p < 7; ++p) {
+    chol_panel(sm, S, NS, p * 64, 7 - p, IDS + (size_t)p * 4096, WS + (size_t)p * 4096,
+               LS, IDS + (size_t)(p + 1) * 4096, WS + (size_t)(p + 1) * 4096);
+    gbar(bar, &phase);
+  }
+
+  for (int idx = gix; idx < NS * NS; idx += gsz) {
+    int i = idx >> 9, j = idx & 511;
+    int d = i >> 6;
+    ILS[idx] = ((j >> 6) == d) ? IDS[(size_t)d * 4096 + (i & 63) * 64 + (j & 63)] : 0.0;
+  }
+  gbar(bar, &phase);
+  for (int lv = 0; lv < 3; ++lv) {
+    int half = 64 << lv, pairs = NS / (2 * half), hb = half >> 6;
+    int tiles = pairs * hb * hb;
+    for (int t = bid; t < tiles; t += nbk) {
+      int p = t / (hb * hb), rem = t % (hb * hb), bi = rem / hb, bj = rem % hb;
+      int base = p * 2 * half;
+      dgemm_nn_core(sm, LS + (size_t)(base + half + bi * 64) * NS + base, NS,
+                    ILS + (size_t)base * NS + base + bj * 64, NS,
+                    TINV + (size_t)p * half * half + (size_t)bi * 64 * half + bj * 64, half,
+                    0, half, 1.0);
+    }
+    gbar(bar, &phase);
+    for (int t = bid; t < tiles; t += nbk) {
+      int p = t / (hb * hb), rem = t % (hb * hb), bi = rem / hb, bj = rem % hb;
+      int base = p * 2 * half;
+      dgemm_nn_core(sm, ILS + (size_t)(base + half + bi * 64) * NS + base + half, NS,
+                    TINV + (size_t)p * half * half + bj * 64, half,
+                    ILS + (size_t)(base + half + bi * 64) * NS + base + bj * 64, NS,
+                    0, half, -1.0);
+    }
+    gbar(bar, &phase);
+  }
+
+  for (int a = bid; a < NS; a += nbk)
+    for (int c = tid; c < NXC; c += 256) {
+      double v = 0.0;
+      if (a < NAR) {
+        if (c < 600) v = TA[(size_t)(400 + c) * NS + a];
+        else if (c < 1106) v = (a == (c - 600)) ? 1.0 : 0.0;
+      }
+      X12[(size_t)a * NXC + c] = v;
+    }
+  gbar(bar, &phase);
+  for (int t = bid; t < 8 * 18; t += nbk) {
+    int bi = t / 18, bj = t % 18;
+    dgemm_nn_core(sm, ILS + (size_t)bi * 64 * NS, NS, X12 + bj * 64, NXC,
+                  XB + (size_t)bi * 64 * NXC + bj * 64, NXC, 0, (bi + 1) * 64, 1.0);
+  }
+  gbar(bar, &phase);
+  for (int t = bid; t < 8 * 18; t += nbk) {
+    int bi = t / 18, bj = t % 18;
+    dgemm_tn_core(sm, ILS + bi * 64, NS, XB + bj * 64, NXC,
+                  X12 + (size_t)bi * 64 * NXC + bj * 64, NXC, bi * 64, NS, 1.0);
+  }
+  gbar(bar, &phase);
+
+  for (int t = bid; t < 16 * 18; t += nbk) gemmM_tile(sm, TA, X12, qv, rv, MRAW, t);
+  gbar(bar, &phase);
+
+  for (int o = bid; o < NG; o += nbk)
+    for (int j2 = tid; j2 < LDMA; j2 += 256) {
+      float v = 0.f;
+      if (j2 < 600) {
+        v = MRAW[(size_t)o * NXC + j2];
+        if (o == 400 + j2) v += 1.0f;
+        if (j2 >= 594) v += MRAW[(size_t)o * NXC + 1100 + (j2 - 594)];
+      } else if (j2 < 1100) {
+        v = MRAW[(size_t)o * NXC + j2];
+      }
+      MALL[(size_t)o * LDMA + j2] = v;
     }
 }
 
@@ -703,52 +764,16 @@
   double* TB   = (double*)(w + OFF_TB);
   double* TINV = (double*)(w + OFF_TINV);
   double* XB   = (double*)(w + OFF_XB);
+  unsigned int* BAR = (unsigned int*)(w + OFF_BAR);
 
   k_build_C<<<dim3(8, NCRP), 256, 0, stream>>>(ud, yd, C);
-  k_gram<<<dim3(24, 48), 256, 0, stream>>>(C, GCC);
-  k_copyG<<<dim3(NG * NG / 256), 256, 0, stream>>>(GCC, qv, rv, G);
-  k_copyTA<<<dim3(NG * NS / 256), 256, 0, stream>>>(GCC, TA);
-
-  k_potrf_inv0<<<1, 256, 0, stream>>>(G, NG, LG, IDG, WG);
-  for (int p = 0; p < 15; ++p) {
-    int nb = 15 - p;
-    k_chol_fused<<<dim3(nb * (nb + 1) / 2), 256, 0, stream>>>(
-        G, NG, p * 64, IDG + (size_t)p * 4096, WG + (size_t)p * 4096, LG,
-        IDG + (size_t)(p + 1) * 4096, WG + (size_t)(p + 1) * 4096);
-  }
-
-  k_init_iL<<<dim3(NG * NG / 256), 256, 0, stream>>>(ILG, 10, IDG);
-  for (int lv = 0; lv < 4; ++lv) {
-    int half = 64 << lv, pairs = NG / (2 * half);
-    dim3 gt(half / 64, half / 64, pairs);
-    k_ilv_tmp<<<gt, 256, 0, stream>>>(LG, NG, ILG, NG, TINV, half);
-    k_ilv_fin<<<gt, 256, 0, stream>>>(ILG, NG, TINV, half);
-  }
-  k_dgemm_nn<<<dim3(NS / 64, NG / 64), 256, 0, stream>>>(ILG, NG, TA, NS, TB, NS, NG, 1, 1.0);
-  k_dgemm_tn<<<dim3(NS / 64, NG / 64), 256, 0, stream>>>(ILG, NG, TB, NS, TA, NS, NG, 1, 1.0);
-
-  k_buildS<<<dim3(8, 8), 256, 0, stream>>>(GCC, TA, S);
-  k_potrf_inv0<<<1, 256, 0, stream>>>(S, NS, LS, IDS, WS);
-  for (int p = 0; p < 7; ++p) {
-    int nb = 7 - p;
-    k_chol_fused<<<dim3(nb * (nb + 1) / 2), 256, 0, stream>>>(
-        S, NS, p * 64, IDS + (size_t)p * 4096, WS + (size_t)p * 4096, LS,
-        IDS + (size_t)(p + 1) * 4096, WS + (size_t)(p + 1) * 4096);
-  }
-  k_init_iL<<<dim3(NS * NS / 256), 256, 0, stream>>>(ILS, 9, IDS);
-  for (int lv = 0; lv < 3; ++lv) {
-    int half = 64 << lv, pairs = NS / (2 * half);
-    dim3 gt(half / 64, half / 64, pairs);
-    k_ilv_tmp<<<gt, 256, 0, stream>>>(LS, NS, ILS, NS, TINV, half);
-    k_ilv_fin<<<gt, 256, 0, stream>>>(ILS, NS, TINV, half);
-  }
-
-  k_build_x12rhs<<<dim3(5, NS), 256, 0, stream>>>(TA, X12);
-  k_dgemm_nn<<<dim3(NXC / 64, NS / 64), 256, 0, stream>>>(ILS, NS, X12, NXC, XB, NXC, NS, 1, 1.0);
-  k_dgemm_tn<<<dim3(NXC / 64, NS / 64), 256, 0, stream>>>(ILS, NS, XB, NXC, X12, NXC, NS, 1, 1.0);
-
-  k_gemm_M<<<dim3(NXC / 64, NG / 64), 256, 0, stream>>>(TA, X12, qv, rv, MRAW);
-  k_assemble_M<<<dim3(5, NG), 256, 0, stream>>>(MRAW, MALL);
+  k_gram<<<dim3(24, 24), 256, 0, stream>>>(C, GCC);
+  hipMemsetAsync(BAR, 0, 64, stream);
+
+  k_coop<<<dim3(NBLK), dim3(256), 0, stream>>>(
+      GCC, G, TA, S, X12, MRAW, MALL, ILG, ILS, IDG, IDS,
+      WG, WS, LG, LS, TB, TINV, XB, qv, rv, BAR);
+
   k_transpose_in<<<dim3(NBATCH / 32, LDMA / 32), 256, 0, stream>>>(ref, ui, yi, INA);
   k_gemm_out<<<dim3(NBATCH / 128, NG / 128), 256, 0, stream>>>(MALL, INA, out);
 }
```

Result: slower. 13.61 ms (+131.2%).
